# Kernel tuning notes

Hardware: AMD Instinct MI355X
Metric: run time of the kernel (lower is better)

The kernel has to match this reference:

```python
import jax, jax.numpy as jnp
import numpy as np

B, T, C = 2, 2048, 2048
H, KVH, D = 32, 8, 64  # num_heads, num_kv_heads, head_dim
G = H // KVH           # queries per kv head


def setup_inputs() -> dict:
    key = jax.random.key(0)
    ks = jax.random.split(key, 6)
    x = jax.random.normal(ks[0], (B, T, C), dtype=jnp.float32)
    # realistic RoPE tables: [T, D], first half = freqs, second half repeats
    inv_freq = 1.0 / (10000.0 ** (np.arange(0, D, 2, dtype=np.float32) / D))
    t = np.arange(T, dtype=np.float32)
    freqs = np.outer(t, inv_freq)               # [T, D/2]
    emb = np.concatenate([freqs, freqs], axis=-1)  # [T, D]
    cos = jnp.asarray(np.cos(emb), dtype=jnp.float32)
    sin = jnp.asarray(np.sin(emb), dtype=jnp.float32)
    # causal mask: True = masked
    mask = jnp.triu(jnp.ones((T, T), dtype=jnp.bool_), k=1)[None, None]  # [1,1,T,T]
    # nn.Linear weights stored as [out, in]
    s = 1.0 / np.sqrt(C)
    Wq = jax.random.uniform(ks[1], (C, C), jnp.float32, -s, s)
    Wk = jax.random.uniform(ks[2], (KVH * D, C), jnp.float32, -s, s)
    Wv = jax.random.uniform(ks[3], (KVH * D, C), jnp.float32, -s, s)
    Wo = jax.random.uniform(ks[4], (C, C), jnp.float32, -s, s)
    return {"x": x, "Wq": Wq, "Wk": Wk, "Wv": Wv, "Wo": Wo,
            "cos": cos, "sin": sin, "mask": mask}


def rotate_half(x):
    x1, x2 = x[..., : D // 2], x[..., D // 2:]
    return jnp.concatenate([-x2, x1], axis=-1)


def reference(x, Wq, Wk, Wv, Wo, cos, sin, mask):
    # projections (nn.Linear: y = x @ W.T)
    q = (x @ Wq.T).reshape(B, T, H, D).transpose(0, 2, 1, 3)    # [B,H,T,D]
    k = (x @ Wk.T).reshape(B, T, KVH, D).transpose(0, 2, 1, 3)  # [B,KVH,T,D]
    v = (x @ Wv.T).reshape(B, T, KVH, D).transpose(0, 2, 1, 3)
    # RoPE (cos/sin broadcast [T,D] -> [B,H,T,D])
    q = q * cos + rotate_half(q) * sin
    k = k * cos + rotate_half(k) * sin
    # GQA: repeat_interleave kv heads
    k = jnp.repeat(k, G, axis=1)  # [B,H,T,D]
    v = jnp.repeat(v, G, axis=1)
    scale = 1.0 / jnp.sqrt(jnp.float32(D))
    attn = jnp.einsum('bhqd,bhkd->bhqk', q, k) * scale  # [B,H,T,T]
    attn = jnp.where(mask, -jnp.inf, attn)
    attn = jax.nn.softmax(attn.astype(jnp.float32), axis=-1).astype(q.dtype)
    out = jnp.einsum('bhqk,bhkd->bhqd', attn, v)  # [B,H,T,D]
    out = out.transpose(0, 2, 1, 3).reshape(B, T, C)
    return out @ Wo.T
```

## Files before the change

### kernel.cpp

```cpp
#include <hip/hip_runtime.h>
#include <hip/hip_bf16.h>
#include <type_traits>

#define T_LEN 2048
#define HN 32
#define KVHN 8

typedef unsigned short u16;
typedef unsigned int u32;
typedef __attribute__((ext_vector_type(8))) short bf16x8;
typedef __attribute__((ext_vector_type(4))) float f32x4;
typedef __attribute__((ext_vector_type(16))) float f32x16;

__device__ __forceinline__ u16 f2b(float f) {
  __hip_bfloat16 h = __float2bfloat16(f);
  return __builtin_bit_cast(u16, h);
}
__device__ __forceinline__ float b2f(u16 u) {
  return __bfloat162float(__builtin_bit_cast(__hip_bfloat16, u));
}
__device__ __forceinline__ u32 pk2(float a, float b) {
  return (u32)f2b(a) | ((u32)f2b(b) << 16);
}
__device__ __forceinline__ float fexp2(float x) {
  float r;
  asm("v_exp_f32 %0, %1" : "=v"(r) : "v"(x));
  return r;
}

__device__ __forceinline__ void gload_lds16(const void* g, void* l) {
  __builtin_amdgcn_global_load_lds(
      (const __attribute__((address_space(1))) u32*)g,
      (__attribute__((address_space(3))) u32*)l, 16, 0, 0);
}

__global__ __launch_bounds__(256) void cvt_all(const float* __restrict__ x,
                                               const float* __restrict__ Wq,
                                               const float* __restrict__ Wk,
                                               const float* __restrict__ Wv,
                                               const float* __restrict__ Wo,
                                               u16* __restrict__ xb, u16* __restrict__ wqb,
                                               u16* __restrict__ wkb, u16* __restrict__ wvb,
                                               u16* __restrict__ wob) {
  int i = blockIdx.x * 256 + threadIdx.x;
  const float* src;
  u16* dst;
  int off;
  if (i < 1048576)      { src = x;  dst = xb;  off = i; }
  else if (i < 1572864) { src = Wq; dst = wqb; off = i - 1048576; }
  else if (i < 1703936) { src = Wk; dst = wkb; off = i - 1572864; }
  else if (i < 1835008) { src = Wv; dst = wvb; off = i - 1703936; }
  else                  { src = Wo; dst = wob; off = i - 1835008; }
  float4 a = ((const float4*)src)[off * 2];
  float4 b = ((const float4*)src)[off * 2 + 1];
  union { u16 s[8]; uint4 v; } r;
  r.s[0] = f2b(a.x); r.s[1] = f2b(a.y); r.s[2] = f2b(a.z); r.s[3] = f2b(a.w);
  r.s[4] = f2b(b.x); r.s[5] = f2b(b.y); r.s[6] = f2b(b.z); r.s[7] = f2b(b.w);
  ((uint4*)dst)[off] = r.v;
}

template <int MODE>
__device__ __forceinline__ void gemm_bt_core(const u16* __restrict__ A,
                                             const u16* __restrict__ Bt,
                                             void* __restrict__ Cv,
                                             const float* __restrict__ cosT,
                                             const float* __restrict__ sinT, float mul,
                                             int brow, int bcol, int N, int K,
                                             u16* As, u16* Bs) {
  int tid = threadIdx.x;
  int w = tid >> 6, l = tid & 63;
  int wr = w >> 1, wc = w & 1;
  int lr = tid >> 2, lc = (tid & 3) * 8;
  f32x4 acc[4][4] = {};
  for (int k0 = 0; k0 < K; k0 += 32) {
    __syncthreads();
#pragma unroll
    for (int i = 0; i < 2; ++i) {
      gload_lds16(A + (size_t)(brow + i * 64 + lr) * K + k0 + lc,
                  (char*)As + i * 4096 + w * 1024);
      gload_lds16(Bt + (size_t)(bcol + i * 64 + lr) * K + k0 + lc,
                  (char*)Bs + i * 4096 + w * 1024);
    }
    __syncthreads();
    bf16x8 af[4], bfr[4];
#pragma unroll
    for (int m = 0; m < 4; ++m)
      af[m] = *(const bf16x8*)((const char*)As + (wr * 64 + m * 16 + (l & 15)) * 64 + (l >> 4) * 16);
#pragma unroll
    for (int n = 0; n < 4; ++n)
      bfr[n] = *(const bf16x8*)((const char*)Bs + (wc * 64 + n * 16 + (l & 15)) * 64 + (l >> 4) * 16);
#pragma unroll
    for (int m = 0; m < 4; ++m)
#pragma unroll
      for (int n = 0; n < 4; ++n)
        acc[m][n] = __builtin_amdgcn_mfma_f32_16x16x32_bf16(af[m], bfr[n], acc[m][n], 0, 0, 0);
  }
  if constexpr (MODE == 2) {
    u16* C = (u16*)Cv;
#pragma unroll
    for (int m = 0; m < 4; ++m)
#pragma unroll
      for (int n = 0; n < 2; ++n)
#pragma unroll
        for (int r = 0; r < 4; ++r) {
          int row = brow + wr * 64 + m * 16 + (l >> 4) * 4 + r;
          int t = row & (T_LEN - 1);
          int dlo = n * 16 + (l & 15);
          float c = cosT[t * 64 + dlo];
          float s = sinT[t * 64 + dlo];
          float lo = acc[m][n][r], hh = acc[m][n + 2][r];
          size_t base = (size_t)row * N + bcol + wc * 64 + n * 16 + (l & 15);
          C[base]      = f2b((lo * c - hh * s) * mul);
          C[base + 32] = f2b((hh * c + lo * s) * mul);
        }
  } else {
#pragma unroll
    for (int m = 0; m < 4; ++m)
#pragma unroll
      for (int n = 0; n < 4; ++n)
#pragma unroll
        for (int r = 0; r < 4; ++r) {
          size_t row = brow + wr * 64 + m * 16 + (l >> 4) * 4 + r;
          size_t col = bcol + wc * 64 + n * 16 + (l & 15);
          if constexpr (MODE == 1)
            ((float*)Cv)[row * N + col] = acc[m][n][r];
          else
            ((u16*)Cv)[row * N + col] = f2b(acc[m][n][r]);
        }
  }
}

template <int MODE>
__global__ __launch_bounds__(256) void gemm_bt(const u16* __restrict__ A,
                                               const u16* __restrict__ Bt,
                                               void* __restrict__ C,
                                               const float* __restrict__ cosT,
                                               const float* __restrict__ sinT,
                                               float mul, int N, int K) {
  __shared__ u16 As[128 * 32];
  __shared__ u16 Bs[128 * 32];
  gemm_bt_core<MODE>(A, Bt, C, cosT, sinT, mul, blockIdx.y * 128, blockIdx.x * 128, N, K, As, Bs);
}

__global__ __launch_bounds__(256) void gemm_qkv(const u16* __restrict__ A,
                                                const u16* __restrict__ Wq,
                                                const u16* __restrict__ Wk,
                                                const u16* __restrict__ Wv,
                                                u16* __restrict__ Qo,
                                                u16* __restrict__ Ko,
                                                u16* __restrict__ Vo,
                                                const float* __restrict__ cosT,
                                                const float* __restrict__ sinT) {
  __shared__ u16 As[128 * 32];
  __shared__ u16 Bs[128 * 32];
  int bx = blockIdx.x, brow = blockIdx.y * 128;
  if (bx < 16)
    gemm_bt_core<2>(A, Wq, Qo, cosT, sinT, 0.125f, brow, bx * 128, 2048, 2048, As, Bs);
  else if (bx < 20)
    gemm_bt_core<2>(A, Wk, Ko, cosT, sinT, 1.0f, brow, (bx - 16) * 128, 512, 2048, As, Bs);
  else
    gemm_bt_core<0>(A, Wv, Vo, nullptr, nullptr, 0.f, brow, (bx - 20) * 128, 512, 2048, As, Bs);
}

#define MKFRAG(SS, RB, OUTV)                                              \
  {                                                                       \
    u32 a_ = pk2(SS[RB + 0], SS[RB + 1]);                                 \
    u32 b_ = pk2(SS[RB + 4], SS[RB + 5]);                                 \
    u32 c_ = pk2(SS[RB + 2], SS[RB + 3]);                                 \
    u32 d_ = pk2(SS[RB + 6], SS[RB + 7]);                                 \
    asm volatile("v_permlane32_swap_b32 %0, %1" : "+v"(a_), "+v"(b_));    \
    asm volatile("v_permlane32_swap_b32 %0, %1" : "+v"(c_), "+v"(d_));    \
    union { u32 u[4]; bf16x8 v; } r_;                                     \
    r_.u[0] = a_; r_.u[1] = c_; r_.u[2] = b_; r_.u[3] = d_;               \
    OUTV = r_.v;                                                          \
  }

__device__ void attn_one(int qi, int h, int kvh, size_t bT,
                         const u16* __restrict__ Q, const u16* __restrict__ K,
                         const u16* __restrict__ V, u16* __restrict__ O,
                         char* lds) {
  const float L2E = 1.4426950408889634f;
  int tid = threadIdx.x;
  int w = tid >> 6, l = tid & 63;
  int lq = l & 31;
  int hi = l >> 5;
  int q0blk = qi * 128;
  int q0w = q0blk + w * 32;
  int nt = 2 * qi + 2;

#pragma unroll
  for (int i = 0; i < 4; ++i) {
    int u = (i * 4 + w) * 64 + l;
    int row = u >> 3, blk = (u & 7) ^ (row & 7);
    gload_lds16(Q + ((bT + q0blk + row) * HN + h) * 64 + blk * 8,
                lds + (i * 4 + w) * 1024);
  }
  __syncthreads();
  bf16x8 qf[4];
  {
    int R = w * 32 + lq;
#pragma unroll
    for (int ks = 0; ks < 4; ++ks) {
      int kb = 2 * ks + hi;
      qf[ks] = *(const bf16x8*)(lds + R * 128 + ((kb ^ (R & 7)) * 16));
    }
  }
  __syncthreads();

  int r2 = tid >> 3;
  int d0v = (tid & 7) * 8;
  uint4 va, vb;

  {
#pragma unroll
    for (int i = 0; i < 2; ++i) {
      int u = (w * 2 + i) * 64 + l;
      int row = u >> 3, blk = (u & 7) ^ (row & 7);
      gload_lds16(K + ((bT + row) * KVHN + kvh) * 64 + blk * 8,
                  lds + (w * 2 + i) * 1024);
    }
    const u16* g0 = V + ((bT + 2 * r2) * KVHN + kvh) * 64 + d0v;
    va = *(const uint4*)g0;
    vb = *(const uint4*)(g0 + KVHN * 64);
    u32* vt = (u32*)(lds + 16384);
    const u16* pa = (const u16*)&va;
    const u16* pb = (const u16*)&vb;
#pragma unroll
    for (int j = 0; j < 8; ++j)
      vt[(d0v + j) * 34 + r2] = (u32)pa[j] | ((u32)pb[j] << 16);
  }

  f32x16 o0 = {}, o1 = {};
  float mx = -1e30f, ls = 0.f;

  for (int t = 0; t < nt; ++t) {
    __syncthreads();
    int cur = t & 1, nxt = cur ^ 1;
    bool last = (t + 1 >= nt);
    int kv0 = t * 64;
    bool skip = kv0 > q0w + 31;

    if (!last) {
      int kvn = kv0 + 64;
#pragma unroll
      for (int i = 0; i < 2; ++i) {
        int u = (w * 2 + i) * 64 + l;
        int row = u >> 3, blk = (u & 7) ^ (row & 7);
        gload_lds16(K + ((bT + kvn + row) * KVHN + kvh) * 64 + blk * 8,
                    lds + nxt * 8192 + (w * 2 + i) * 1024);
      }
      const u16* g0 = V + ((bT + kvn + 2 * r2) * KVHN + kvh) * 64 + d0v;
      va = *(const uint4*)g0;
      vb = *(const uint4*)(g0 + KVHN * 64);
    }

    f32x16 s0 = {}, s1 = {};
    if (!skip) {
      const char* kb = lds + cur * 8192;
      __builtin_amdgcn_s_setprio(1);
#pragma unroll
      for (int ks = 0; ks < 4; ++ks) {
        int kbi = 2 * ks + hi;
        int R0 = lq, R1 = 32 + lq;
        bf16x8 k0 = *(const bf16x8*)(kb + R0 * 128 + ((kbi ^ (R0 & 7)) * 16));
        bf16x8 k1 = *(const bf16x8*)(kb + R1 * 128 + ((kbi ^ (R1 & 7)) * 16));
        s0 = __builtin_amdgcn_mfma_f32_32x32x16_bf16(k0, qf[ks], s0, 0, 0, 0);
        s1 = __builtin_amdgcn_mfma_f32_32x32x16_bf16(k1, qf[ks], s1, 0, 0, 0);
      }
      __builtin_amdgcn_s_setprio(0);
      if (kv0 + 63 > q0w) {
        int qa = q0w + lq;
#pragma unroll
        for (int r = 0; r < 16; ++r) {
          int kvl = (r & 3) + 8 * (r >> 2) + 4 * hi;
          if (kv0 + kvl > qa) s0[r] = -1e30f;
          if (kv0 + 32 + kvl > qa) s1[r] = -1e30f;
        }
      }
      float rm = s0[0];
#pragma unroll
      for (int r = 1; r < 16; ++r) rm = fmaxf(rm, s0[r]);
#pragma unroll
      for (int r = 0; r < 16; ++r) rm = fmaxf(rm, s1[r]);
      rm = fmaxf(rm, __shfl_xor(rm, 32));
      float nm = mx;
      if (!__all(rm <= mx + 8.0f)) {
        nm = fmaxf(mx, rm);
        float fac = fexp2((mx - nm) * L2E);
        mx = nm;
        ls *= fac;
#pragma unroll
        for (int r = 0; r < 16; ++r) { o0[r] *= fac; o1[r] *= fac; }
      }
      float psum = 0.f;
#pragma unroll
      for (int r = 0; r < 16; ++r) { float p = fexp2((s0[r] - nm) * L2E); s0[r] = p; psum += p; }
#pragma unroll
      for (int r = 0; r < 16; ++r) { float p = fexp2((s1[r] - nm) * L2E); s1[r] = p; psum += p; }
      ls += psum;
    }

    if (!last) {
      u32* vt = (u32*)(lds + 16384 + nxt * 8704);
      const u16* pa = (const u16*)&va;
      const u16* pb = (const u16*)&vb;
#pragma unroll
      for (int j = 0; j < 8; ++j)
        vt[(d0v + j) * 34 + r2] = (u32)pa[j] | ((u32)pb[j] << 16);
    }

    if (!skip) {
      const u32* vt = (const u32*)(lds + 16384 + cur * 8704);
#pragma unroll
      for (int sl = 0; sl < 4; ++sl) {
        bf16x8 paf;
        if (sl == 0)      MKFRAG(s0, 0, paf)
        else if (sl == 1) MKFRAG(s0, 8, paf)
        else if (sl == 2) MKFRAG(s1, 0, paf)
        else              MKFRAG(s1, 8, paf)
        int m0 = 8 * sl + 4 * hi;
        __builtin_amdgcn_s_setprio(1);
#pragma unroll
        for (int g = 0; g < 2; ++g) {
          int d = lq + 32 * g;
          const u32* vp = vt + d * 34 + m0;
          union { u32 u[4]; bf16x8 v; } vv;
          uint2 lo = *(const uint2*)vp;
          uint2 hi2 = *(const uint2*)(vp + 2);
          vv.u[0] = lo.x; vv.u[1] = lo.y; vv.u[2] = hi2.x; vv.u[3] = hi2.y;
          if (g == 0) o0 = __builtin_amdgcn_mfma_f32_32x32x16_bf16(vv.v, paf, o0, 0, 0, 0);
          else        o1 = __builtin_amdgcn_mfma_f32_32x32x16_bf16(vv.v, paf, o1, 0, 0, 0);
        }
        __builtin_amdgcn_s_setprio(0);
      }
    }
  }

  __syncthreads();
  ls += __shfl_xor(ls, 32);
  float inv = 1.f / ls;
  char* od = lds + w * 4096;
#pragma unroll
  for (int g = 0; g < 2; ++g) {
#pragma unroll
    for (int r = 0; r < 16; r += 2) {
      int d = (r & 3) + 8 * (r >> 2) + 4 * hi + 32 * g;
      float e0 = (g ? o1[r] : o0[r]) * inv;
      float e1 = (g ? o1[r + 1] : o0[r + 1]) * inv;
      *(u32*)(od + lq * 128 + ((d * 2) ^ ((lq & 7) << 4))) = pk2(e0, e1);
    }
  }
  __syncthreads();
#pragma unroll
  for (int i = 0; i < 4; ++i) {
    int q = l >> 1;
    int c = (l & 1) * 4 + i;
    uint4 vv = *(const uint4*)(od + q * 128 + ((c * 16) ^ ((q & 7) << 4)));
    *(uint4*)(O + ((bT + q0w + q) * HN + h) * 64 + c * 8) = vv;
  }
}

__global__ __launch_bounds__(256, 3) void attn_kernel(const u16* __restrict__ Q,
                                                      const u16* __restrict__ K,
                                                      const u16* __restrict__ V,
                                                      u16* __restrict__ O) {
  int qp = blockIdx.x, h = blockIdx.y, b = blockIdx.z;
  int kvh = h >> 2;
  const size_t bT = (size_t)b * T_LEN;
  __shared__ char lds[33792];

  attn_one(qp, h, kvh, bT, Q, K, V, O, lds);
  __syncthreads();
  attn_one(15 - qp, h, kvh, bT, Q, K, V, O, lds);
}

extern "C" void kernel_launch(void* const* d_in, const int* in_sizes, int n_in,
                              void* d_out, int out_size, void* d_ws, size_t ws_size,
                              hipStream_t stream) {
  const float* x    = (const float*)d_in[0];
  const float* Wq   = (const float*)d_in[1];
  const float* Wk   = (const float*)d_in[2];
  const float* Wv   = (const float*)d_in[3];
  const float* Wo   = (const float*)d_in[4];
  const float* cosT = (const float*)d_in[5];
  const float* sinT = (const float*)d_in[6];

  char* ws = (char*)d_ws;
  u16* xb  = (u16*)(ws + 0);
  u16* wqb = (u16*)(ws + 16777216);
  u16* wkb = (u16*)(ws + 25165824);
  u16* wvb = (u16*)(ws + 27262976);
  u16* wob = (u16*)(ws + 29360128);
  u16* qb  = (u16*)(ws + 37748736);
  u16* kb  = (u16*)(ws + 54525952);
  u16* vb  = (u16*)(ws + 58720256);
  u16* aob = (u16*)(ws + 62914560);

  cvt_all<<<9216, 256, 0, stream>>>(x, Wq, Wk, Wv, Wo, xb, wqb, wkb, wvb, wob);

  gemm_qkv<<<dim3(24, 32), 256, 0, stream>>>(xb, wqb, wkb, wvb, qb, kb, vb, cosT, sinT);

  attn_kernel<<<dim3(8, 32, 2), 256, 0, stream>>>(qb, kb, vb, aob);

  gemm_bt<1><<<dim3(16, 32), 256, 0, stream>>>(aob, wob, d_out, nullptr, nullptr, 0.f, 2048, 2048);
}
```

Baseline: 227.0 us.

## Fuse paired causal query blocks into one KV sweep sharing K/V tiles

Measured after the change: 226.5 us. About the same (-0.2%).

```diff
diff --git a/kernel.cpp b/kernel.cpp
--- a/kernel.cpp
+++ b/kernel.cpp
@@ -20,7 +20,9 @@
   return __bfloat162float(__builtin_bit_cast(__hip_bfloat16, u));
 }
 __device__ __forceinline__ u32 pk2(float a, float b) {
-  return (u32)f2b(a) | ((u32)f2b(b) << 16);
+  u32 r;
+  asm("v_cvt_pk_bf16_f32 %0, %1, %2" : "=v"(r) : "v"(a), "v"(b));
+  return r;
 }
 __device__ __forceinline__ float fexp2(float x) {
   float r;
@@ -155,7 +157,7 @@
   __shared__ u16 Bs[128 * 32];
   int bx = blockIdx.x, brow = blockIdx.y * 128;
   if (bx < 16)
-    gemm_bt_core<2>(A, Wq, Qo, cosT, sinT, 0.125f, brow, bx * 128, 2048, 2048, As, Bs);
+    gemm_bt_core<2>(A, Wq, Qo, cosT, sinT, 0.18033688f, brow, bx * 128, 2048, 2048, As, Bs);
   else if (bx < 20)
     gemm_bt_core<2>(A, Wk, Ko, cosT, sinT, 1.0f, brow, (bx - 16) * 128, 512, 2048, As, Bs);
   else
@@ -175,34 +177,172 @@
     OUTV = r_.v;                                                          \
   }
 
-__device__ void attn_one(int qi, int h, int kvh, size_t bT,
-                         const u16* __restrict__ Q, const u16* __restrict__ K,
-                         const u16* __restrict__ V, u16* __restrict__ O,
-                         char* lds) {
-  const float L2E = 1.4426950408889634f;
+#define SIDE_S(QF, Q0, MX, LS, O0, O1)                                    \
+  {                                                                       \
+    s0 = (f32x16){}; s1 = (f32x16){};                                     \
+    const char* kbuf = lds + cur * 8192;                                  \
+    __builtin_amdgcn_s_setprio(1);                                        \
+    _Pragma("unroll")                                                     \
+    for (int ks = 0; ks < 4; ++ks) {                                      \
+      int kbi = 2 * ks + hi;                                              \
+      int R0 = lq, R1 = 32 + lq;                                          \
+      bf16x8 k0 = *(const bf16x8*)(kbuf + R0 * 128 + ((kbi ^ (R0 & 7)) * 16)); \
+      bf16x8 k1 = *(const bf16x8*)(kbuf + R1 * 128 + ((kbi ^ (R1 & 7)) * 16)); \
+      s0 = __builtin_amdgcn_mfma_f32_32x32x16_bf16(k0, QF[ks], s0, 0, 0, 0); \
+      s1 = __builtin_amdgcn_mfma_f32_32x32x16_bf16(k1, QF[ks], s1, 0, 0, 0); \
+    }                                                                     \
+    __builtin_amdgcn_s_setprio(0);                                        \
+    if (kv0 + 63 > Q0) {                                                  \
+      int qa = Q0 + lq;                                                   \
+      _Pragma("unroll")                                                   \
+      for (int r = 0; r < 16; ++r) {                                      \
+        int kvl = (r & 3) + 8 * (r >> 2) + 4 * hi;                        \
+        if (kv0 + kvl > qa) s0[r] = -1e30f;                               \
+        if (kv0 + 32 + kvl > qa) s1[r] = -1e30f;                          \
+      }                                                                   \
+    }                                                                     \
+    float a0 = fmaxf(s0[0], s1[0]);                                       \
+    float a1 = fmaxf(s0[1], s1[1]);                                       \
+    float a2 = fmaxf(s0[2], s1[2]);                                       \
+    float a3 = fmaxf(s0[3], s1[3]);                                       \
+    _Pragma("unroll")                                                     \
+    for (int r = 4; r < 16; r += 4) {                                     \
+      a0 = fmaxf(fmaxf(s0[r], s1[r]), a0);                                \
+      a1 = fmaxf(fmaxf(s0[r + 1], s1[r + 1]), a1);                        \
+      a2 = fmaxf(fmaxf(s0[r + 2], s1[r + 2]), a2);                        \
+      a3 = fmaxf(fmaxf(s0[r + 3], s1[r + 3]), a3);                        \
+    }                                                                     \
+    float rm = fmaxf(fmaxf(a0, a1), fmaxf(a2, a3));                       \
+    rm = fmaxf(rm, __shfl_xor(rm, 32));                                   \
+    float nm = MX;                                                        \
+    if (!__all(rm <= MX + 8.0f)) {                                        \
+      nm = fmaxf(MX, rm);                                                 \
+      float fac = fexp2(MX - nm);                                         \
+      MX = nm;                                                            \
+      LS *= fac;                                                          \
+      _Pragma("unroll")                                                   \
+      for (int r = 0; r < 16; ++r) { O0[r] *= fac; O1[r] *= fac; }        \
+    }                                                                     \
+    float p0 = 0.f, p1 = 0.f, p2 = 0.f, p3 = 0.f;                         \
+    _Pragma("unroll")                                                     \
+    for (int r = 0; r < 16; r += 4) {                                     \
+      p0 += (s0[r]     = fexp2(s0[r]     - nm));                          \
+      p1 += (s0[r + 1] = fexp2(s0[r + 1] - nm));                          \
+      p2 += (s0[r + 2] = fexp2(s0[r + 2] - nm));                          \
+      p3 += (s0[r + 3] = fexp2(s0[r + 3] - nm));                          \
+    }                                                                     \
+    _Pragma("unroll")                                                     \
+    for (int r = 0; r < 16; r += 4) {                                     \
+      p0 += (s1[r]     = fexp2(s1[r]     - nm));                          \
+      p1 += (s1[r + 1] = fexp2(s1[r + 1] - nm));                          \
+      p2 += (s1[r + 2] = fexp2(s1[r + 2] - nm));                          \
+      p3 += (s1[r + 3] = fexp2(s1[r + 3] - nm));                          \
+    }                                                                     \
+    LS += (p0 + p1) + (p2 + p3);                                          \
+  }
+
+#define SIDE_PV(O0, O1)                                                   \
+  {                                                                       \
+    const u32* vt = (const u32*)(lds + 16384 + cur * 8704);               \
+    _Pragma("unroll")                                                     \
+    for (int sl = 0; sl < 4; ++sl) {                                      \
+      bf16x8 paf;                                                         \
+      if (sl == 0)      MKFRAG(s0, 0, paf)                                \
+      else if (sl == 1) MKFRAG(s0, 8, paf)                                \
+      else if (sl == 2) MKFRAG(s1, 0, paf)                                \
+      else              MKFRAG(s1, 8, paf)                                \
+      int m0 = 8 * sl + 4 * hi;                                           \
+      __builtin_amdgcn_s_setprio(1);                                      \
+      _Pragma("unroll")                                                   \
+      for (int g = 0; g < 2; ++g) {                                       \
+        int d = lq + 32 * g;                                              \
+        const u32* vp = vt + d * 34 + m0;                                 \
+        union { u32 u[4]; bf16x8 v; } vv;                                 \
+        uint2 lo = *(const uint2*)vp;                                     \
+        uint2 hi2 = *(const uint2*)(vp + 2);                              \
+        vv.u[0] = lo.x; vv.u[1] = lo.y; vv.u[2] = hi2.x; vv.u[3] = hi2.y; \
+        if (g == 0) O0 = __builtin_amdgcn_mfma_f32_32x32x16_bf16(vv.v, paf, O0, 0, 0, 0); \
+        else        O1 = __builtin_amdgcn_mfma_f32_32x32x16_bf16(vv.v, paf, O1, 0, 0, 0); \
+      }                                                                   \
+      __builtin_amdgcn_s_setprio(0);                                      \
+    }                                                                     \
+  }
+
+#define SIDE_STORE(O0, O1, LS, Q0)                                        \
+  {                                                                       \
+    float lsum = LS + __shfl_xor(LS, 32);                                 \
+    float inv = 1.f / lsum;                                               \
+    char* od = lds + w * 4096;                                            \
+    _Pragma("unroll")                                                     \
+    for (int g = 0; g < 2; ++g) {                                         \
+      _Pragma("unroll")                                                   \
+      for (int r = 0; r < 16; r += 2) {                                   \
+        int d = (r & 3) + 8 * (r >> 2) + 4 * hi + 32 * g;                 \
+        float e0 = (g ? O1[r] : O0[r]) * inv;                             \
+        float e1 = (g ? O1[r + 1] : O0[r + 1]) * inv;                     \
+        *(u32*)(od + lq * 128 + ((d * 2) ^ ((lq & 7) << 4))) = pk2(e0, e1); \
+      }                                                                   \
+    }                                                                     \
+    __syncthreads();                                                      \
+    _Pragma("unroll")                                                     \
+    for (int i = 0; i < 4; ++i) {                                         \
+      int q = l >> 1;                                                     \
+      int c = (l & 1) * 4 + i;                                            \
+      uint4 vv = *(const uint4*)(od + q * 128 + ((c * 16) ^ ((q & 7) << 4))); \
+      *(uint4*)(O + ((bT + Q0 + q) * HN + h) * 64 + c * 8) = vv;          \
+    }                                                                     \
+  }
+
+__global__ __launch_bounds__(256, 3) void attn_kernel(const u16* __restrict__ Q,
+                                                      const u16* __restrict__ K,
+                                                      const u16* __restrict__ V,
+                                                      u16* __restrict__ O) {
+  int qp = blockIdx.x, h = blockIdx.y, b = blockIdx.z;
+  int kvh = h >> 2;
+  const size_t bT = (size_t)b * T_LEN;
+  __shared__ char lds[33792];
+
   int tid = threadIdx.x;
   int w = tid >> 6, l = tid & 63;
   int lq = l & 31;
   int hi = l >> 5;
-  int q0blk = qi * 128;
-  int q0w = q0blk + w * 32;
-  int nt = 2 * qi + 2;
-
+  int qiL = qp, qiH = 15 - qp;
+  int q0L = qiL * 128 + w * 32;
+  int q0H = qiH * 128 + w * 32;
+  int nt = 2 * qiH + 2;
+
+  bf16x8 qfL[4], qfH[4];
 #pragma unroll
   for (int i = 0; i < 4; ++i) {
     int u = (i * 4 + w) * 64 + l;
     int row = u >> 3, blk = (u & 7) ^ (row & 7);
-    gload_lds16(Q + ((bT + q0blk + row) * HN + h) * 64 + blk * 8,
+    gload_lds16(Q + ((bT + qiL * 128 + row) * HN + h) * 64 + blk * 8,
                 lds + (i * 4 + w) * 1024);
   }
   __syncthreads();
-  bf16x8 qf[4];
   {
     int R = w * 32 + lq;
 #pragma unroll
     for (int ks = 0; ks < 4; ++ks) {
       int kb = 2 * ks + hi;
-      qf[ks] = *(const bf16x8*)(lds + R * 128 + ((kb ^ (R & 7)) * 16));
+      qfL[ks] = *(const bf16x8*)(lds + R * 128 + ((kb ^ (R & 7)) * 16));
+    }
+  }
+  __syncthreads();
+#pragma unroll
+  for (int i = 0; i < 4; ++i) {
+    int u = (i * 4 + w) * 64 + l;
+    int row = u >> 3, blk = (u & 7) ^ (row & 7);
+    gload_lds16(Q + ((bT + qiH * 128 + row) * HN + h) * 64 + blk * 8,
+                lds + (i * 4 + w) * 1024);
+  }
+  __syncthreads();
+  {
+    int R = w * 32 + lq;
+#pragma unroll
+    for (int ks = 0; ks < 4; ++ks) {
+      int kb = 2 * ks + hi;
+      qfH[ks] = *(const bf16x8*)(lds + R * 128 + ((kb ^ (R & 7)) * 16));
     }
   }
   __syncthreads();
@@ -230,15 +370,16 @@
       vt[(d0v + j) * 34 + r2] = (u32)pa[j] | ((u32)pb[j] << 16);
   }
 
-  f32x16 o0 = {}, o1 = {};
-  float mx = -1e30f, ls = 0.f;
+  f32x16 oL0 = {}, oL1 = {}, oH0 = {}, oH1 = {};
+  float mxL = -1e30f, lsL = 0.f, mxH = -1e30f, lsH = 0.f;
 
   for (int t = 0; t < nt; ++t) {
     __syncthreads();
     int cur = t & 1, nxt = cur ^ 1;
     bool last = (t + 1 >= nt);
     int kv0 = t * 64;
-    bool skip = kv0 > q0w + 31;
+    bool actL = (kv0 <= q0L + 31);
+    bool actH = (kv0 <= q0H + 31);
 
     if (!last) {
       int kvn = kv0 + 64;
@@ -254,51 +395,8 @@
       vb = *(const uint4*)(g0 + KVHN * 64);
     }
 
-    f32x16 s0 = {}, s1 = {};
-    if (!skip) {
-      const char* kb = lds + cur * 8192;
-      __builtin_amdgcn_s_setprio(1);
-#pragma unroll
-      for (int ks = 0; ks < 4; ++ks) {
-        int kbi = 2 * ks + hi;
-        int R0 = lq, R1 = 32 + lq;
-        bf16x8 k0 = *(const bf16x8*)(kb + R0 * 128 + ((kbi ^ (R0 & 7)) * 16));
-        bf16x8 k1 = *(const bf16x8*)(kb + R1 * 128 + ((kbi ^ (R1 & 7)) * 16));
-        s0 = __builtin_amdgcn_mfma_f32_32x32x16_bf16(k0, qf[ks], s0, 0, 0, 0);
-        s1 = __builtin_amdgcn_mfma_f32_32x32x16_bf16(k1, qf[ks], s1, 0, 0, 0);
-      }
-      __builtin_amdgcn_s_setprio(0);
-      if (kv0 + 63 > q0w) {
-        int qa = q0w + lq;
-#pragma unroll
-        for (int r = 0; r < 16; ++r) {
-          int kvl = (r & 3) + 8 * (r >> 2) + 4 * hi;
-          if (kv0 + kvl > qa) s0[r] = -1e30f;
-          if (kv0 + 32 + kvl > qa) s1[r] = -1e30f;
-        }
-      }
-      float rm = s0[0];
-#pragma unroll
-      for (int r = 1; r < 16; ++r) rm = fmaxf(rm, s0[r]);
-#pragma unroll
-      for (int r = 0; r < 16; ++r) rm = fmaxf(rm, s1[r]);
-      rm = fmaxf(rm, __shfl_xor(rm, 32));
-      float nm = mx;
-      if (!__all(rm <= mx + 8.0f)) {
-        nm = fmaxf(mx, rm);
-        float fac = fexp2((mx - nm) * L2E);
-        mx = nm;
-        ls *= fac;
-#pragma unroll
-        for (int r = 0; r < 16; ++r) { o0[r] *= fac; o1[r] *= fac; }
-      }
-      float psum = 0.f;
-#pragma unroll
-      for (int r = 0; r < 16; ++r) { float p = fexp2((s0[r] - nm) * L2E); s0[r] = p; psum += p; }
-#pragma unroll
-      for (int r = 0; r < 16; ++r) { float p = fexp2((s1[r] - nm) * L2E); s1[r] = p; psum += p; }
-      ls += psum;
-    }
+    f32x16 s0, s1;
+    if (actL) SIDE_S(qfL, q0L, mxL, lsL, oL0, oL1)
 
     if (!last) {
       u32* vt = (u32*)(lds + 16384 + nxt * 8704);
@@ -309,69 +407,18 @@
         vt[(d0v + j) * 34 + r2] = (u32)pa[j] | ((u32)pb[j] << 16);
     }
 
-    if (!skip) {
-      const u32* vt = (const u32*)(lds + 16384 + cur * 8704);
-#pragma unroll
-      for (int sl = 0; sl < 4; ++sl) {
-        bf16x8 paf;
-        if (sl == 0)      MKFRAG(s0, 0, paf)
-        else if (sl == 1) MKFRAG(s0, 8, paf)
-        else if (sl == 2) MKFRAG(s1, 0, paf)
-        else              MKFRAG(s1, 8, paf)
-        int m0 = 8 * sl + 4 * hi;
-        __builtin_amdgcn_s_setprio(1);
-#pragma unroll
-        for (int g = 0; g < 2; ++g) {
-          int d = lq + 32 * g;
-          const u32* vp = vt + d * 34 + m0;
-          union { u32 u[4]; bf16x8 v; } vv;
-          uint2 lo = *(const uint2*)vp;
-          uint2 hi2 = *(const uint2*)(vp + 2);
-          vv.u[0] = lo.x; vv.u[1] = lo.y; vv.u[2] = hi2.x; vv.u[3] = hi2.y;
-          if (g == 0) o0 = __builtin_amdgcn_mfma_f32_32x32x16_bf16(vv.v, paf, o0, 0, 0, 0);
-          else        o1 = __builtin_amdgcn_mfma_f32_32x32x16_bf16(vv.v, paf, o1, 0, 0, 0);
-        }
-        __builtin_amdgcn_s_setprio(0);
-      }
-    }
-  }
-
-  __syncthreads();
-  ls += __shfl_xor(ls, 32);
-  float inv = 1.f / ls;
-  char* od = lds + w * 4096;
-#pragma unroll
-  for (int g = 0; g < 2; ++g) {
-#pragma unroll
-    for (int r = 0; r < 16; r += 2) {
-      int d = (r & 3) + 8 * (r >> 2) + 4 * hi + 32 * g;
-      float e0 = (g ? o1[r] : o0[r]) * inv;
-      float e1 = (g ? o1[r + 1] : o0[r + 1]) * inv;
-      *(u32*)(od + lq * 128 + ((d * 2) ^ ((lq & 7) << 4))) = pk2(e0, e1);
-    }
-  }
-  __syncthreads();
-#pragma unroll
-  for (int i = 0; i < 4; ++i) {
-    int q = l >> 1;
-    int c = (l & 1) * 4 + i;
-    uint4 vv = *(const uint4*)(od + q * 128 + ((c * 16) ^ ((q & 7) << 4)));
-    *(uint4*)(O + ((bT + q0w + q) * HN + h) * 64 + c * 8) = vv;
-  }
-}
-
-__global__ __launch_bounds__(256, 3) void attn_kernel(const u16* __restrict__ Q,
-                                                      const u16* __restrict__ K,
-                                                      const u16* __restrict__ V,
-                                                      u16* __restrict__ O) {
-  int qp = blockIdx.x, h = blockIdx.y, b = blockIdx.z;
-  int kvh = h >> 2;
-  const size_t bT = (size_t)b * T_LEN;
-  __shared__ char lds[33792];
-
-  attn_one(qp, h, kvh, bT, Q, K, V, O, lds);
-  __syncthreads();
-  attn_one(15 - qp, h, kvh, bT, Q, K, V, O, lds);
+    if (actL) SIDE_PV(oL0, oL1)
+
+    if (actH) {
+      SIDE_S(qfH, q0H, mxH, lsH, oH0, oH1)
+      SIDE_PV(oH0, oH1)
+    }
+  }
+
+  __syncthreads();
+  SIDE_STORE(oL0, oL1, lsL, q0L)
+  __syncthreads();
+  SIDE_STORE(oH0, oH1, lsH, q0H)
 }
 
 extern "C" void kernel_launch(void* const* d_in, const int* in_sizes, int n_in,
```
